# Optimization experiments

Hardware: AMD Instinct MI355X
Metric: run time of the kernel (lower is better)

The kernel has to match this reference:

```python
import jax, jax.numpy as jnp
import numpy as np

B, S, D = 4, 4096, 2048
E, H, SPE = 64, 1024, 1
NUM_SLOTS = E * SPE
TEMP = 1.0


def setup_inputs() -> dict:
    key = jax.random.key(0)
    ks = jax.random.split(key, 6)
    x = jax.random.normal(ks[0], (B, S, D), dtype=jnp.float32)
    W_disp = jax.random.normal(ks[1], (NUM_SLOTS, D), dtype=jnp.float32) * 0.02
    # torch Linear default init ~ U(-1/sqrt(fan_in), 1/sqrt(fan_in))
    W1 = jax.random.uniform(ks[2], (E, H, D), jnp.float32, -1.0, 1.0) / np.sqrt(D)
    b1 = jax.random.uniform(ks[3], (E, H), jnp.float32, -1.0, 1.0) / np.sqrt(D)
    W2 = jax.random.uniform(ks[4], (E, D, H), jnp.float32, -1.0, 1.0) / np.sqrt(H)
    b2 = jax.random.uniform(ks[5], (E, D), jnp.float32, -1.0, 1.0) / np.sqrt(H)
    return {"x": x, "W_disp": W_disp, "W1": W1, "b1": b1, "W2": W2, "b2": b2}


def reference(x, W_disp, W1, b1, W2, b2):
    # eval mode: dropout inactive, no calibration, z_loss_weight=0
    Bb, Ss, Dd = x.shape
    xf = x.reshape(-1, Dd)                       # (T, D)
    logits = (xf @ W_disp.T) / TEMP              # (T, num_slots)
    dispatch = jax.nn.softmax(logits, axis=0)    # softmax over tokens (T > 1)
    combine = jax.nn.softmax(logits, axis=-1)    # softmax over slots
    slot_inputs = dispatch.T @ xf                # (num_slots, D)
    x_exp = slot_inputs.reshape(E, SPE, Dd)      # (E, S_per, D)
    h = jnp.einsum('esd,ehd->esh', x_exp, W1) + b1[:, None, :]
    h = jax.nn.gelu(h, approximate=False)        # torch F.gelu is exact (erf)
    out = jnp.einsum('esh,edh->esd', h, W2) + b2[:, None, :]
    slot_outputs = out.reshape(NUM_SLOTS, Dd)
    y = combine @ slot_outputs                   # (T, D)
    return y.reshape(Bb, Ss, Dd)
```

## Files before the change

### kernel.cpp

```cpp
#include <hip/hip_runtime.h>
#include <math.h>

#define T_TOK 16384
#define D_DIM 2048
#define NSLOT 64
#define H_DIM 1024

__global__ __launch_bounds__(256) void k_logits(const float* __restrict__ x,
                                                const float* __restrict__ Wd,
                                                float* __restrict__ logits) {
    __shared__ float xs[32][68];
    __shared__ float ws[64][68];
    const int tid = threadIdx.x;
    const int tblk = blockIdx.x * 32;
    const int sb = tid & 15;
    const int t0 = (tid >> 4) * 2;
    float acc[2][4] = {};

    for (int k0 = 0; k0 < D_DIM; k0 += 64) {
        #pragma unroll
        for (int i = 0; i < 2; ++i) {
            int fi = tid + i * 256;
            int r = fi >> 4, c4 = fi & 15;
            *(float4*)&xs[r][c4 * 4] =
                *(const float4*)&x[(size_t)(tblk + r) * D_DIM + k0 + c4 * 4];
        }
        #pragma unroll
        for (int i = 0; i < 4; ++i) {
            int fi = tid + i * 256;
            int r = fi >> 4, c4 = fi & 15;
            *(float4*)&ws[r][c4 * 4] =
                *(const float4*)&Wd[(size_t)r * D_DIM + k0 + c4 * 4];
        }
        __syncthreads();
        #pragma unroll
        for (int k = 0; k < 64; k += 4) {
            float4 xv[2], wv[4];
            #pragma unroll
            for (int i = 0; i < 2; ++i) xv[i] = *(const float4*)&xs[t0 + i][k];
            #pragma unroll
            for (int j = 0; j < 4; ++j) wv[j] = *(const float4*)&ws[sb + j * 16][k];
            #pragma unroll
            for (int i = 0; i < 2; ++i)
                #pragma unroll
                for (int j = 0; j < 4; ++j)
                    acc[i][j] += xv[i].x * wv[j].x + xv[i].y * wv[j].y +
                                 xv[i].z * wv[j].z + xv[i].w * wv[j].w;
        }
        __syncthreads();
    }
    #pragma unroll
    for (int i = 0; i < 2; ++i)
        #pragma unroll
        for (int j = 0; j < 4; ++j)
            logits[(size_t)(tblk + t0 + i) * NSLOT + sb + j * 16] = acc[i][j];
}

__global__ __launch_bounds__(256) void k_cred1(const float* __restrict__ logits,
                                               float* __restrict__ pm,
                                               float* __restrict__ pz) {
    __shared__ float lm[256], lz[256];
    const int tid = threadIdx.x;
    const size_t base = (size_t)blockIdx.x * 256 * NSLOT;
    float m = -1e30f, z = 0.f;
    for (int i = 0; i < 64; ++i) {
        float v = logits[base + (size_t)i * 256 + tid];
        float nm = fmaxf(m, v);
        z = z * __expf(m - nm) + __expf(v - nm);
        m = nm;
    }
    lm[tid] = m; lz[tid] = z;
    __syncthreads();
    if (tid < 64) {
        float M = lm[tid], Z = lz[tid];
        #pragma unroll
        for (int i = 1; i < 4; ++i) {
            float m2 = lm[tid + i * 64], z2 = lz[tid + i * 64];
            float nm = fmaxf(M, m2);
            Z = Z * __expf(M - nm) + z2 * __expf(m2 - nm);
            M = nm;
        }
        pm[blockIdx.x * NSLOT + tid] = M;
        pz[blockIdx.x * NSLOT + tid] = Z;
    }
}

__global__ void k_cred2(const float* __restrict__ pm, const float* __restrict__ pz,
                        float* __restrict__ m_out, float* __restrict__ invZ_out) {
    const int s = threadIdx.x;
    float M = -1e30f, Z = 0.f;
    for (int i = 0; i < 64; ++i) {
        float m2 = pm[i * NSLOT + s], z2 = pz[i * NSLOT + s];
        float nm = fmaxf(M, m2);
        Z = Z * __expf(M - nm) + z2 * __expf(m2 - nm);
        M = nm;
    }
    m_out[s] = M;
    invZ_out[s] = 1.f / Z;
}

__global__ __launch_bounds__(256) void k_slot_inputs(const float* __restrict__ x,
        const float* __restrict__ logits, const float* __restrict__ mS,
        const float* __restrict__ invZ, float* __restrict__ partial) {
    __shared__ float xs[64][128];
    __shared__ float pls[64][64];
    __shared__ float ms[64], zs[64];
    const int tid = threadIdx.x;
    const int d0 = blockIdx.x * 128;
    const int tc0 = blockIdx.y * 512;
    if (tid < 64) { ms[tid] = mS[tid]; zs[tid] = invZ[tid]; }
    const int g = tid & 31;
    const int s0 = (tid >> 5) * 8;
    float4 acc[8] = {};

    for (int sub = 0; sub < 8; ++sub) {
        const int t0 = tc0 + sub * 64;
        __syncthreads();
        #pragma unroll
        for (int i = 0; i < 8; ++i) {
            int fi = tid + i * 256;
            int r = fi >> 5, c4 = fi & 31;
            *(float4*)&xs[r][c4 * 4] =
                *(const float4*)&x[(size_t)(t0 + r) * D_DIM + d0 + c4 * 4];
        }
        #pragma unroll
        for (int i = 0; i < 16; ++i) {
            int fi = tid + i * 256;
            int r = fi >> 6, s = fi & 63;
            float lv = logits[(size_t)(t0 + r) * NSLOT + s];
            pls[r][s] = __expf(lv - ms[s]) * zs[s];
        }
        __syncthreads();
        for (int t = 0; t < 64; ++t) {
            float4 xv = *(const float4*)&xs[t][g * 4];
            #pragma unroll
            for (int i = 0; i < 8; ++i) {
                float p = pls[t][s0 + i];
                acc[i].x += p * xv.x; acc[i].y += p * xv.y;
                acc[i].z += p * xv.z; acc[i].w += p * xv.w;
            }
        }
    }
    #pragma unroll
    for (int i = 0; i < 8; ++i) {
        int s = s0 + i;
        *(float4*)&partial[((size_t)blockIdx.y * NSLOT + s) * D_DIM + d0 + g * 4] = acc[i];
    }
}

__global__ __launch_bounds__(256) void k_sred(const float* __restrict__ partial,
                                              float* __restrict__ slot_in) {
    const int idx = blockIdx.x * 256 + threadIdx.x;
    float4 a = {0.f, 0.f, 0.f, 0.f};
    for (int c = 0; c < 32; ++c) {
        float4 v = *(const float4*)&partial[(size_t)c * (NSLOT * D_DIM) + (size_t)idx * 4];
        a.x += v.x; a.y += v.y; a.z += v.z; a.w += v.w;
    }
    *(float4*)&slot_in[(size_t)idx * 4] = a;
}

__global__ __launch_bounds__(256) void k_mlp1(const float* __restrict__ W1,
                                              const float* __restrict__ b1,
                                              const float* __restrict__ slot_in,
                                              float* __restrict__ h) {
    const int wave = threadIdx.x >> 6, lane = threadIdx.x & 63;
    const int row = blockIdx.x * 4 + wave;
    const int e = row >> 10;
    const float* wr = W1 + (size_t)row * D_DIM;
    const float* xr = slot_in + (size_t)e * D_DIM;
    float acc = 0.f;
    #pragma unroll
    for (int i = 0; i < 8; ++i) {
        int k = (lane + i * 64) * 4;
        float4 w4 = *(const float4*)(wr + k);
        float4 x4 = *(const float4*)(xr + k);
        acc += w4.x * x4.x + w4.y * x4.y + w4.z * x4.z + w4.w * x4.w;
    }
    #pragma unroll
    for (int off = 32; off; off >>= 1) acc += __shfl_xor(acc, off);
    if (lane == 0) {
        float v = acc + b1[row];
        h[row] = 0.5f * v * (1.f + erff(v * 0.70710678118654752f));
    }
}

__global__ __launch_bounds__(256) void k_mlp2(const float* __restrict__ W2,
                                              const float* __restrict__ b2,
                                              const float* __restrict__ h,
                                              float* __restrict__ slot_out) {
    const int wave = threadIdx.x >> 6, lane = threadIdx.x & 63;
    const int row = blockIdx.x * 4 + wave;
    const int e = row >> 11;
    const float* wr = W2 + (size_t)row * H_DIM;
    const float* xr = h + (size_t)e * H_DIM;
    float acc = 0.f;
    #pragma unroll
    for (int i = 0; i < 4; ++i) {
        int k = (lane + i * 64) * 4;
        float4 w4 = *(const float4*)(wr + k);
        float4 x4 = *(const float4*)(xr + k);
        acc += w4.x * x4.x + w4.y * x4.y + w4.z * x4.z + w4.w * x4.w;
    }
    #pragma unroll
    for (int off = 32; off; off >>= 1) acc += __shfl_xor(acc, off);
    if (lane == 0) slot_out[row] = acc + b2[row];
}

__global__ __launch_bounds__(256) void k_combine(const float* __restrict__ logits,
                                                 const float* __restrict__ so,
                                                 float* __restrict__ y) {
    __shared__ float cl[64][65];
    __shared__ float sol[64][128];
    const int tid = threadIdx.x;
    const int d0 = blockIdx.x * 128;
    const int tb = blockIdx.y * 64;
    #pragma unroll
    for (int i = 0; i < 16; ++i) {
        int fi = tid + i * 256;
        int r = fi >> 6, s = fi & 63;
        cl[r][s] = logits[(size_t)(tb + r) * NSLOT + s];
    }
    #pragma unroll
    for (int i = 0; i < 8; ++i) {
        int fi = tid + i * 256;
        int r = fi >> 5, c4 = fi & 31;
        *(float4*)&sol[r][c4 * 4] =
            *(const float4*)&so[(size_t)r * D_DIM + d0 + c4 * 4];
    }
    __syncthreads();
    if (tid < 64) {
        float M = -1e30f;
        for (int s = 0; s < 64; ++s) M = fmaxf(M, cl[tid][s]);
        float Z = 0.f;
        for (int s = 0; s < 64; ++s) { float e = __expf(cl[tid][s] - M); cl[tid][s] = e; Z += e; }
        float r = 1.f / Z;
        for (int s = 0; s < 64; ++s) cl[tid][s] *= r;
    }
    __syncthreads();
    const int g0 = tid & 15;
    const int t0 = (tid >> 4) * 4;
    float4 acc[4][2] = {};
    for (int s = 0; s < 64; ++s) {
        float4 sv[2];
        float cv[4];
        #pragma unroll
        for (int j = 0; j < 2; ++j) sv[j] = *(const float4*)&sol[s][(g0 + j * 16) * 4];
        #pragma unroll
        for (int i = 0; i < 4; ++i) cv[i] = cl[t0 + i][s];
        #pragma unroll
        for (int i = 0; i < 4; ++i)
            #pragma unroll
            for (int j = 0; j < 2; ++j) {
                acc[i][j].x += cv[i] * sv[j].x; acc[i][j].y += cv[i] * sv[j].y;
                acc[i][j].z += cv[i] * sv[j].z; acc[i][j].w += cv[i] * sv[j].w;
            }
    }
    #pragma unroll
    for (int i = 0; i < 4; ++i)
        #pragma unroll
        for (int j = 0; j < 2; ++j)
            *(float4*)&y[(size_t)(tb + t0 + i) * D_DIM + d0 + (g0 + j * 16) * 4] = acc[i][j];
}

extern "C" void kernel_launch(void* const* d_in, const int* in_sizes, int n_in,
                              void* d_out, int out_size, void* d_ws, size_t ws_size,
                              hipStream_t stream) {
    const float* x  = (const float*)d_in[0];
    const float* Wd = (const float*)d_in[1];
    const float* W1 = (const float*)d_in[2];
    const float* b1 = (const float*)d_in[3];
    const float* W2 = (const float*)d_in[4];
    const float* b2 = (const float*)d_in[5];
    float* y = (float*)d_out;

    float* w = (float*)d_ws;
    float* logits  = w;
    float* pm      = logits + (size_t)T_TOK * NSLOT;
    float* pz      = pm + 64 * NSLOT;
    float* mS      = pz + 64 * NSLOT;
    float* invZ    = mS + NSLOT;
    float* partial = invZ + NSLOT;
    float* slot_in = partial + (size_t)32 * NSLOT * D_DIM;
    float* h       = slot_in + (size_t)NSLOT * D_DIM;
    float* slot_out= h + (size_t)NSLOT * H_DIM;

    k_logits<<<T_TOK / 32, 256, 0, stream>>>(x, Wd, logits);
    k_cred1<<<64, 256, 0, stream>>>(logits, pm, pz);
    k_cred2<<<1, 64, 0, stream>>>(pm, pz, mS, invZ);
    k_slot_inputs<<<dim3(16, 32), 256, 0, stream>>>(x, logits, mS, invZ, partial);
    k_sred<<<128, 256, 0, stream>>>(partial, slot_in);
    k_mlp1<<<(NSLOT * H_DIM) / 4, 256, 0, stream>>>(W1, b1, slot_in, h);
    k_mlp2<<<(NSLOT * D_DIM) / 4, 256, 0, stream>>>(W2, b2, h, slot_out);
    k_combine<<<dim3(16, 256), 256, 0, stream>>>(logits, slot_out, y);
}
```

Baseline: 444.4 us.

## Retile logits with split-K, precompute softmax probs, enlarge slot-input and combine tiles

The logits GEMM now uses 256-token tiles with an 8x8 register block, XOR-swizzled shared memory and an 8-way split over D, followed by a reduction kernel. A new kernel computes the dispatch and combine probabilities once per token. The slot-input and combine kernels then read those precomputed values instead of recomputing exps, and use larger per-thread tiles. The cost is extra launches and extra global traffic for the split-K partials and the probability buffers.

After: 509.5 us. 14.7% more time.

```diff
diff --git a/kernel.cpp b/kernel.cpp
--- a/kernel.cpp
+++ b/kernel.cpp
@@ -5,55 +5,73 @@
 #define D_DIM 2048
 #define NSLOT 64
 #define H_DIM 1024
+#define KSPLIT 8
+#define KCH (D_DIM / KSPLIT)
 
 __global__ __launch_bounds__(256) void k_logits(const float* __restrict__ x,
                                                 const float* __restrict__ Wd,
-                                                float* __restrict__ logits) {
-    __shared__ float xs[32][68];
-    __shared__ float ws[64][68];
+                                                float* __restrict__ plog) {
+    __shared__ float xs[256][32];
+    __shared__ float ws[64][32];
     const int tid = threadIdx.x;
-    const int tblk = blockIdx.x * 32;
-    const int sb = tid & 15;
-    const int t0 = (tid >> 4) * 2;
-    float acc[2][4] = {};
-
-    for (int k0 = 0; k0 < D_DIM; k0 += 64) {
-        #pragma unroll
-        for (int i = 0; i < 2; ++i) {
-            int fi = tid + i * 256;
-            int r = fi >> 4, c4 = fi & 15;
-            *(float4*)&xs[r][c4 * 4] =
-                *(const float4*)&x[(size_t)(tblk + r) * D_DIM + k0 + c4 * 4];
-        }
-        #pragma unroll
-        for (int i = 0; i < 4; ++i) {
-            int fi = tid + i * 256;
-            int r = fi >> 4, c4 = fi & 15;
-            *(float4*)&ws[r][c4 * 4] =
-                *(const float4*)&Wd[(size_t)r * D_DIM + k0 + c4 * 4];
-        }
+    const int tblk = blockIdx.x * 256;
+    const int ks = blockIdx.y;
+    const int koff = ks * KCH;
+    const int tq = tid >> 3;
+    const int sg = tid & 7;
+    float acc[8][8] = {};
+
+    for (int kc = 0; kc < KCH; kc += 32) {
         __syncthreads();
         #pragma unroll
-        for (int k = 0; k < 64; k += 4) {
-            float4 xv[2], wv[4];
+        for (int ii = 0; ii < 8; ++ii) {
+            int fi = tid + ii * 256;
+            int t = fi >> 3, c = fi & 7;
+            *(float4*)&xs[t][(c ^ (t & 7)) << 2] =
+                *(const float4*)&x[(size_t)(tblk + t) * D_DIM + koff + kc + c * 4];
+        }
+        #pragma unroll
+        for (int ii = 0; ii < 2; ++ii) {
+            int fi = tid + ii * 256;
+            int s = fi >> 3, c = fi & 7;
+            *(float4*)&ws[s][(c ^ (s & 7)) << 2] =
+                *(const float4*)&Wd[(size_t)s * D_DIM + koff + kc + c * 4];
+        }
+        __syncthreads();
+        #pragma unroll
+        for (int c = 0; c < 8; ++c) {
+            float4 wv[8];
             #pragma unroll
-            for (int i = 0; i < 2; ++i) xv[i] = *(const float4*)&xs[t0 + i][k];
+            for (int j = 0; j < 8; ++j)
+                wv[j] = *(const float4*)&ws[sg + 8 * j][(c ^ sg) << 2];
             #pragma unroll
-            for (int j = 0; j < 4; ++j) wv[j] = *(const float4*)&ws[sb + j * 16][k];
-            #pragma unroll
-            for (int i = 0; i < 2; ++i)
+            for (int i = 0; i < 8; ++i) {
+                float4 xv = *(const float4*)&xs[tq + 32 * i][(c ^ (tq & 7)) << 2];
                 #pragma unroll
-                for (int j = 0; j < 4; ++j)
-                    acc[i][j] += xv[i].x * wv[j].x + xv[i].y * wv[j].y +
-                                 xv[i].z * wv[j].z + xv[i].w * wv[j].w;
-        }
-        __syncthreads();
-    }
-    #pragma unroll
-    for (int i = 0; i < 2; ++i)
-        #pragma unroll
-        for (int j = 0; j < 4; ++j)
-            logits[(size_t)(tblk + t0 + i) * NSLOT + sb + j * 16] = acc[i][j];
+                for (int j = 0; j < 8; ++j)
+                    acc[i][j] += xv.x * wv[j].x + xv.y * wv[j].y +
+                                 xv.z * wv[j].z + xv.w * wv[j].w;
+            }
+        }
+    }
+    #pragma unroll
+    for (int i = 0; i < 8; ++i)
+        #pragma unroll
+        for (int j = 0; j < 8; ++j)
+            plog[((size_t)ks * T_TOK + tblk + tq + 32 * i) * NSLOT + sg + 8 * j] =
+                acc[i][j];
+}
+
+__global__ __launch_bounds__(256) void k_lsum(const float* __restrict__ plog,
+                                              float* __restrict__ logits) {
+    const size_t idx = ((size_t)blockIdx.x * 256 + threadIdx.x) * 4;
+    float4 a = *(const float4*)&plog[idx];
+    #pragma unroll
+    for (int j = 1; j < KSPLIT; ++j) {
+        float4 v = *(const float4*)&plog[(size_t)j * T_TOK * NSLOT + idx];
+        a.x += v.x; a.y += v.y; a.z += v.z; a.w += v.w;
+    }
+    *(float4*)&logits[idx] = a;
 }
 
 __global__ __launch_bounds__(256) void k_cred1(const float* __restrict__ logits,
@@ -99,64 +117,84 @@
     invZ_out[s] = 1.f / Z;
 }
 
+__global__ __launch_bounds__(256) void k_probs(const float* __restrict__ logits,
+                                               const float* __restrict__ mS,
+                                               const float* __restrict__ invZ,
+                                               float* __restrict__ disp,
+                                               float* __restrict__ comb) {
+    const int wave = threadIdx.x >> 6, lane = threadIdx.x & 63;
+    const int t = blockIdx.x * 4 + wave;
+    float v = logits[(size_t)t * NSLOT + lane];
+    float M = v;
+    #pragma unroll
+    for (int off = 32; off; off >>= 1) M = fmaxf(M, __shfl_xor(M, off));
+    float e = __expf(v - M);
+    float Z = e;
+    #pragma unroll
+    for (int off = 32; off; off >>= 1) Z += __shfl_xor(Z, off);
+    comb[(size_t)t * NSLOT + lane] = e / Z;
+    disp[(size_t)t * NSLOT + lane] = __expf(v - mS[lane]) * invZ[lane];
+}
+
 __global__ __launch_bounds__(256) void k_slot_inputs(const float* __restrict__ x,
-        const float* __restrict__ logits, const float* __restrict__ mS,
-        const float* __restrict__ invZ, float* __restrict__ partial) {
-    __shared__ float xs[64][128];
-    __shared__ float pls[64][64];
-    __shared__ float ms[64], zs[64];
+        const float* __restrict__ disp, float* __restrict__ partial) {
+    __shared__ float xs[32][256];
+    __shared__ float pls[32][64];
     const int tid = threadIdx.x;
-    const int d0 = blockIdx.x * 128;
-    const int tc0 = blockIdx.y * 512;
-    if (tid < 64) { ms[tid] = mS[tid]; zs[tid] = invZ[tid]; }
-    const int g = tid & 31;
-    const int s0 = (tid >> 5) * 8;
-    float4 acc[8] = {};
+    const int d0 = blockIdx.x * 256;
+    const int tc0 = blockIdx.y * 256;
+    const int dg = tid & 31;
+    const int sgq = tid >> 5;
+    float4 acc0[8] = {}, acc1[8] = {};
 
     for (int sub = 0; sub < 8; ++sub) {
-        const int t0 = tc0 + sub * 64;
+        const int t0 = tc0 + sub * 32;
         __syncthreads();
         #pragma unroll
-        for (int i = 0; i < 8; ++i) {
-            int fi = tid + i * 256;
-            int r = fi >> 5, c4 = fi & 31;
+        for (int ii = 0; ii < 8; ++ii) {
+            int fi = tid + ii * 256;
+            int r = fi >> 6, c4 = fi & 63;
             *(float4*)&xs[r][c4 * 4] =
                 *(const float4*)&x[(size_t)(t0 + r) * D_DIM + d0 + c4 * 4];
         }
         #pragma unroll
-        for (int i = 0; i < 16; ++i) {
-            int fi = tid + i * 256;
-            int r = fi >> 6, s = fi & 63;
-            float lv = logits[(size_t)(t0 + r) * NSLOT + s];
-            pls[r][s] = __expf(lv - ms[s]) * zs[s];
+        for (int ii = 0; ii < 2; ++ii) {
+            int fi = tid + ii * 256;
+            int r = fi >> 4, s4 = fi & 15;
+            *(float4*)&pls[r][s4 * 4] =
+                *(const float4*)&disp[(size_t)(t0 + r) * NSLOT + s4 * 4];
         }
         __syncthreads();
-        for (int t = 0; t < 64; ++t) {
-            float4 xv = *(const float4*)&xs[t][g * 4];
+        for (int t = 0; t < 32; ++t) {
+            float4 xv0 = *(const float4*)&xs[t][dg * 4];
+            float4 xv1 = *(const float4*)&xs[t][128 + dg * 4];
             #pragma unroll
             for (int i = 0; i < 8; ++i) {
-                float p = pls[t][s0 + i];
-                acc[i].x += p * xv.x; acc[i].y += p * xv.y;
-                acc[i].z += p * xv.z; acc[i].w += p * xv.w;
+                float p = pls[t][sgq * 8 + i];
+                acc0[i].x += p * xv0.x; acc0[i].y += p * xv0.y;
+                acc0[i].z += p * xv0.z; acc0[i].w += p * xv0.w;
+                acc1[i].x += p * xv1.x; acc1[i].y += p * xv1.y;
+                acc1[i].z += p * xv1.z; acc1[i].w += p * xv1.w;
             }
         }
     }
     #pragma unroll
     for (int i = 0; i < 8; ++i) {
-        int s = s0 + i;
-        *(float4*)&partial[((size_t)blockIdx.y * NSLOT + s) * D_DIM + d0 + g * 4] = acc[i];
+        int s = sgq * 8 + i;
+        *(float4*)&partial[((size_t)blockIdx.y * NSLOT + s) * D_DIM + d0 + dg * 4] = acc0[i];
+        *(float4*)&partial[((size_t)blockIdx.y * NSLOT + s) * D_DIM + d0 + 128 + dg * 4] = acc1[i];
     }
 }
 
 __global__ __launch_bounds__(256) void k_sred(const float* __restrict__ partial,
                                               float* __restrict__ slot_in) {
-    const int idx = blockIdx.x * 256 + threadIdx.x;
+    const size_t idx = ((size_t)blockIdx.x * 256 + threadIdx.x) * 4;
     float4 a = {0.f, 0.f, 0.f, 0.f};
-    for (int c = 0; c < 32; ++c) {
-        float4 v = *(const float4*)&partial[(size_t)c * (NSLOT * D_DIM) + (size_t)idx * 4];
+    for (int c = 0; c < 64; ++c) {
+        float4 v = *(const float4*)&partial[(size_t)c * (NSLOT * D_DIM) + idx];
         a.x += v.x; a.y += v.y; a.z += v.z; a.w += v.w;
     }
-    *(float4*)&slot_in[(size_t)idx * 4] = a;
+    *(float4*)&slot_in[idx] = a;
 }
 
 __global__ __launch_bounds__(256) void k_mlp1(const float* __restrict__ W1,
@@ -206,60 +244,49 @@
     if (lane == 0) slot_out[row] = acc + b2[row];
 }
 
-__global__ __launch_bounds__(256) void k_combine(const float* __restrict__ logits,
+__global__ __launch_bounds__(256) void k_combine(const float* __restrict__ comb,
                                                  const float* __restrict__ so,
                                                  float* __restrict__ y) {
-    __shared__ float cl[64][65];
+    __shared__ float cl[128][68];
     __shared__ float sol[64][128];
     const int tid = threadIdx.x;
     const int d0 = blockIdx.x * 128;
-    const int tb = blockIdx.y * 64;
-    #pragma unroll
-    for (int i = 0; i < 16; ++i) {
-        int fi = tid + i * 256;
-        int r = fi >> 6, s = fi & 63;
-        cl[r][s] = logits[(size_t)(tb + r) * NSLOT + s];
-    }
-    #pragma unroll
-    for (int i = 0; i < 8; ++i) {
-        int fi = tid + i * 256;
+    const int tb = blockIdx.y * 128;
+    const int tq = tid >> 4;
+    const int dgq = tid & 15;
+    #pragma unroll
+    for (int ii = 0; ii < 8; ++ii) {
+        int fi = tid + ii * 256;
+        int r = fi >> 4, s4 = fi & 15;
+        *(float4*)&cl[r][s4 * 4] =
+            *(const float4*)&comb[(size_t)(tb + r) * NSLOT + s4 * 4];
+    }
+    #pragma unroll
+    for (int ii = 0; ii < 8; ++ii) {
+        int fi = tid + ii * 256;
         int r = fi >> 5, c4 = fi & 31;
         *(float4*)&sol[r][c4 * 4] =
             *(const float4*)&so[(size_t)r * D_DIM + d0 + c4 * 4];
     }
     __syncthreads();
-    if (tid < 64) {
-        float M = -1e30f;
-        for (int s = 0; s < 64; ++s) M = fmaxf(M, cl[tid][s]);
-        float Z = 0.f;
-        for (int s = 0; s < 64; ++s) { float e = __expf(cl[tid][s] - M); cl[tid][s] = e; Z += e; }
-        float r = 1.f / Z;
-        for (int s = 0; s < 64; ++s) cl[tid][s] *= r;
-    }
-    __syncthreads();
-    const int g0 = tid & 15;
-    const int t0 = (tid >> 4) * 4;
-    float4 acc[4][2] = {};
+    float4 acc0[8] = {}, acc1[8] = {};
     for (int s = 0; s < 64; ++s) {
-        float4 sv[2];
-        float cv[4];
-        #pragma unroll
-        for (int j = 0; j < 2; ++j) sv[j] = *(const float4*)&sol[s][(g0 + j * 16) * 4];
-        #pragma unroll
-        for (int i = 0; i < 4; ++i) cv[i] = cl[t0 + i][s];
-        #pragma unroll
-        for (int i = 0; i < 4; ++i)
-            #pragma unroll
-            for (int j = 0; j < 2; ++j) {
-                acc[i][j].x += cv[i] * sv[j].x; acc[i][j].y += cv[i] * sv[j].y;
-                acc[i][j].z += cv[i] * sv[j].z; acc[i][j].w += cv[i] * sv[j].w;
-            }
-    }
-    #pragma unroll
-    for (int i = 0; i < 4; ++i)
-        #pragma unroll
-        for (int j = 0; j < 2; ++j)
-            *(float4*)&y[(size_t)(tb + t0 + i) * D_DIM + d0 + (g0 + j * 16) * 4] = acc[i][j];
+        float4 sv0 = *(const float4*)&sol[s][dgq * 4];
+        float4 sv1 = *(const float4*)&sol[s][64 + dgq * 4];
+        #pragma unroll
+        for (int i = 0; i < 8; ++i) {
+            float cv = cl[tq + 16 * i][s];
+            acc0[i].x += cv * sv0.x; acc0[i].y += cv * sv0.y;
+            acc0[i].z += cv * sv0.z; acc0[i].w += cv * sv0.w;
+            acc1[i].x += cv * sv1.x; acc1[i].y += cv * sv1.y;
+            acc1[i].z += cv * sv1.z; acc1[i].w += cv * sv1.w;
+        }
+    }
+    #pragma unroll
+    for (int i = 0; i < 8; ++i) {
+        *(float4*)&y[(size_t)(tb + tq + 16 * i) * D_DIM + d0 + dgq * 4] = acc0[i];
+        *(float4*)&y[(size_t)(tb + tq + 16 * i) * D_DIM + d0 + 64 + dgq * 4] = acc1[i];
+    }
 }
 
 extern "C" void kernel_launch(void* const* d_in, const int* in_sizes, int n_in,
@@ -274,22 +301,27 @@
     float* y = (float*)d_out;
 
     float* w = (float*)d_ws;
-    float* logits  = w;
+    float* plog    = w;
+    float* logits  = plog + (size_t)KSPLIT * T_TOK * NSLOT;
     float* pm      = logits + (size_t)T_TOK * NSLOT;
     float* pz      = pm + 64 * NSLOT;
     float* mS      = pz + 64 * NSLOT;
     float* invZ    = mS + NSLOT;
-    float* partial = invZ + NSLOT;
-    float* slot_in = partial + (size_t)32 * NSLOT * D_DIM;
+    float* disp    = invZ + NSLOT;
+    float* comb    = disp + (size_t)T_TOK * NSLOT;
+    float* partial = comb + (size_t)T_TOK * NSLOT;
+    float* slot_in = partial + (size_t)64 * NSLOT * D_DIM;
     float* h       = slot_in + (size_t)NSLOT * D_DIM;
     float* slot_out= h + (size_t)NSLOT * H_DIM;
 
-    k_logits<<<T_TOK / 32, 256, 0, stream>>>(x, Wd, logits);
+    k_logits<<<dim3(T_TOK / 256, KSPLIT), 256, 0, stream>>>(x, Wd, plog);
+    k_lsum<<<(T_TOK * NSLOT) / (4 * 256), 256, 0, stream>>>(plog, logits);
     k_cred1<<<64, 256, 0, stream>>>(logits, pm, pz);
     k_cred2<<<1, 64, 0, stream>>>(pm, pz, mS, invZ);
-    k_slot_inputs<<<dim3(16, 32), 256, 0, stream>>>(x, logits, mS, invZ, partial);
-    k_sred<<<128, 256, 0, stream>>>(partial, slot_in);
+    k_probs<<<T_TOK / 4, 256, 0, stream>>>(logits, mS, invZ, disp, comb);
+    k_slot_inputs<<<dim3(8, 64), 256, 0, stream>>>(x, disp, partial);
+    k_sred<<<(NSLOT * D_DIM) / (4 * 256), 256, 0, stream>>>(partial, slot_in);
     k_mlp1<<<(NSLOT * H_DIM) / 4, 256, 0, stream>>>(W1, b1, slot_in, h);
     k_mlp2<<<(NSLOT * D_DIM) / 4, 256, 0, stream>>>(W2, b2, h, slot_out);
-    k_combine<<<dim3(16, 256), 256, 0, stream>>>(logits, slot_out, y);
-}
+    k_combine<<<dim3(16, 128), 256, 0, stream>>>(comb, slot_out, y);
+}
```
